# Kernel tuning notes

Measured on AMD Instinct MI355X. Metric: run time of the kernel, lower is better.

The kernel has to match this reference:

```python
import jax, jax.numpy as jnp
import numpy as np

B, S, DIN, E, M, L = 16, 4096, 64, 512, 128, 4


def _phi(u, R):
    # u: [B,S,E] (already scaled by E**-0.25), R: [E,M]
    logits = u @ R - 0.5 * jnp.sum(u * u, axis=-1, keepdims=True)
    logits = logits - jax.lax.stop_gradient(jnp.max(logits))  # constant shift cancels in num/den ratio
    return jnp.exp(logits) / np.sqrt(M).astype(np.float32)


def setup_inputs() -> dict:
    key = jax.random.key(0)
    ks = jax.random.split(key, 32)
    n = jax.random.normal
    d = {
        'x': n(ks[0], (B, S, DIN), jnp.float32),
        'Wi': n(ks[1], (DIN, E)) / np.sqrt(DIN),
        'bi': jnp.zeros((E,)),
        'pos': n(ks[2], (S, E)) * 0.02,
        'Wq': n(ks[3], (L, E, E)) / np.sqrt(E),
        'bq': jnp.zeros((L, E)),
        'Wk': n(ks[4], (L, E, E)) / np.sqrt(E),
        'bk': jnp.zeros((L, E)),
        'Wv': n(ks[5], (L, E, E)) / np.sqrt(E),
        'bv': jnp.zeros((L, E)),
        'Wo': n(ks[6], (L, E, E)) / np.sqrt(E),
        'bo': jnp.zeros((L, E)),
        'R': n(ks[7], (L, E, M)),
        'ln_g': jnp.ones((L, E)),
        'ln_b': jnp.zeros((L, E)),
        'W1': n(ks[8], (L, E, 4 * E)) / np.sqrt(E),
        'b1': jnp.zeros((L, 4 * E)),
        'W2': n(ks[9], (L, 4 * E, E)) / np.sqrt(4 * E),
        'b2': jnp.zeros((L, E)),
        'Wr1': n(ks[10], (E, E // 2)) / np.sqrt(E),
        'br1': jnp.zeros((E // 2,)),
        'Wr2': n(ks[11], (E // 2, 1)) / np.sqrt(E // 2),
        'br2': jnp.zeros((1,)),
    }
    return d


def reference(x, Wi, bi, pos, Wq, bq, Wk, bk, Wv, bv, Wo, bo, R, ln_g, ln_b, W1, b1, W2, b2, Wr1, br1, Wr2, br2):
    h = x @ Wi + bi + pos[None, :, :]  # [B,S,E]
    scale = E ** -0.25
    for i in range(L):
        residual = h
        # --- Performer linear attention (non-causal FAVOR+) ---
        q = h @ Wq[i] + bq[i]
        k = h @ Wk[i] + bk[i]
        v = h @ Wv[i] + bv[i]
        pq = _phi(q * scale, R[i])  # [B,S,M]
        pk = _phi(k * scale, R[i])  # [B,S,M]
        kv = jnp.einsum('bsm,bse->bme', pk, v)  # [B,M,E]
        z = jnp.sum(pk, axis=1)                  # [B,M]
        num = jnp.einsum('bsm,bme->bse', pq, kv)
        den = jnp.einsum('bsm,bm->bs', pq, z)[..., None]
        a = (num / (den + 1e-6)) @ Wo[i] + bo[i]
        # --- LayerNorm ---
        mu = jnp.mean(a, axis=-1, keepdims=True)
        var = jnp.var(a, axis=-1, keepdims=True)
        y = (a - mu) * jax.lax.rsqrt(var + 1e-5) * ln_g[i] + ln_b[i]
        # --- FFN (dropout is identity in eval) ---
        ff = jax.nn.gelu(y @ W1[i] + b1[i], approximate=False) @ W2[i] + b2[i]
        h = ff + residual
    pooled = h[:, 0, :]  # [B,E]
    return jax.nn.relu(pooled @ Wr1 + br1) @ Wr2 + br2  # [B,1]
```

## Files before the change

kernel.cpp:

```cpp
#include <hip/hip_runtime.h>
#include <math.h>

static constexpr int  cB   = 16;
static constexpr int  cS   = 4096;
static constexpr int  cDIN = 64;
static constexpr int  cE   = 512;
static constexpr int  cM   = 128;
static constexpr int  cL   = 4;
static constexpr int  cFF  = 2048;
static constexpr int  cHE  = 256;
static constexpr long cNBS = (long)cB * cS;
static constexpr int  cNF  = 1536;

typedef __attribute__((ext_vector_type(8))) short  bf16x8;
typedef __attribute__((ext_vector_type(4))) short  bf16x4;
typedef __attribute__((ext_vector_type(4))) float  f32x4;

typedef const __attribute__((address_space(1))) unsigned int g_u32;
typedef __attribute__((address_space(3))) unsigned int l_u32;

__device__ __forceinline__ float b2f(unsigned short u) {
  union { unsigned int i; float f; } x; x.i = ((unsigned int)u) << 16; return x.f;
}
__device__ __forceinline__ unsigned short f2b(float f) {
  union { float f; unsigned int i; } x; x.f = f;
  unsigned int r = x.i + 0x7FFFu + ((x.i >> 16) & 1u);
  return (unsigned short)(r >> 16);
}

#define PSCALE 0.21022410381342863f
#define PNRM   0.022097086912079608f
#define PINV   0.08838834764831845f

#define FLAG_BIAS    2
#define FLAG_GELU    4
#define FLAG_RES     8
#define FLAG_VT      16
#define FLAG_DEN     32
#define FLAG_RNORM   64
#define FLAG_PHIK    128
#define FLAG_F32OUT  256
#define FLAG_SPLITK8 512
#define FLAG_ATOMIC  1024
#define FLAG_FUSED   2048

#define GMT 128
#define GNT 128
#define GBK 32

__global__ __launch_bounds__(256, 2)
void gemm_kernel(const unsigned short* __restrict__ A,
                 const unsigned short* __restrict__ Bt,
                 const unsigned short* __restrict__ bias,
                 const unsigned short* __restrict__ Res,
                 const float* __restrict__ aux,
                 float* __restrict__ pmax,
                 void* __restrict__ C,
                 int K, int N, int lda, int ldb, float alpha, int flags,
                 long sA, long sB, long sC)
{
  __shared__ __align__(16) unsigned char sraw[18048];
  unsigned short (*As)[32] = (unsigned short (*)[32])sraw;
  unsigned short (*Bs)[32] = (unsigned short (*)[32])(sraw + 8192);
  unsigned short (*stage)[136] = (unsigned short (*)[136])sraw;
  float* wred  = (float*)(sraw + 17472);

  const int tid  = threadIdx.x;
  const int lane = tid & 63;
  const int wid  = tid >> 6;

  int bx = blockIdx.x, by = blockIdx.y;
  if (flags & FLAG_FUSED) { bx = blockIdx.y; by = blockIdx.x; }

  long zb = blockIdx.z;
  const long zc = blockIdx.z;
  int koff = 0;
  if (flags & FLAG_SPLITK8) { koff = (int)(zb & 7) * K; zb >>= 3; }

  const unsigned short* Ab = A + zb * sA + (long)bx * GMT * lda + koff;
  const unsigned short* Bb = Bt + zb * sB + (long)by * GNT * ldb + koff;

  const int srow = wid * 16 + (lane >> 2);
  const int scol = (lane & 3) << 3;
  const unsigned short* gA = Ab + (long)srow * lda + scol;
  const unsigned short* gB = Bb + (long)srow * ldb + scol;
  l_u32* lA0 = (l_u32*)&As[srow][scol];
  l_u32* lA1 = (l_u32*)&As[srow + 64][scol];
  l_u32* lB0 = (l_u32*)&Bs[srow][scol];
  l_u32* lB1 = (l_u32*)&Bs[srow + 64][scol];

  const f32x4 fzero = {0.f, 0.f, 0.f, 0.f};
  f32x4 acc[4][4];
#pragma unroll
  for (int i = 0; i < 4; ++i)
#pragma unroll
    for (int j = 0; j < 4; ++j) acc[i][j] = fzero;

  const int wm = (wid >> 1) << 6;
  const int wn = (wid & 1) << 6;
  const int fm = lane & 15;
  const int kq = (lane >> 4) << 3;

  const long ka64 = (long)64 * lda, kb64 = (long)64 * ldb;
  for (int k0 = 0; k0 < K; k0 += GBK) {
    __builtin_amdgcn_global_load_lds((g_u32*)(gA + k0),        lA0, 16, 0, 0);
    __builtin_amdgcn_global_load_lds((g_u32*)(gA + ka64 + k0), lA1, 16, 0, 0);
    __builtin_amdgcn_global_load_lds((g_u32*)(gB + k0),        lB0, 16, 0, 0);
    __builtin_amdgcn_global_load_lds((g_u32*)(gB + kb64 + k0), lB1, 16, 0, 0);
    __syncthreads();

    bf16x8 af[4], bfv[4];
#pragma unroll
    for (int i = 0; i < 4; ++i) {
      af[i]  = *(const bf16x8*)&As[wm + i * 16 + fm][kq];
      bfv[i] = *(const bf16x8*)&Bs[wn + i * 16 + fm][kq];
    }
#pragma unroll
    for (int i = 0; i < 4; ++i)
#pragma unroll
      for (int j = 0; j < 4; ++j)
        acc[i][j] = __builtin_amdgcn_mfma_f32_16x16x32_bf16(af[i], bfv[j], acc[i][j], 0, 0, 0);
    __syncthreads();
  }

  const int rq = (lane >> 4) << 2;
  const long crow0 = (long)bx * GMT + wm;
  const int  ccol0 = by * GNT + wn;

  long rnoff = 0;
  if (flags & FLAG_FUSED) {
    if (by < 4) flags = FLAG_BIAS | FLAG_VT;
    else { flags = FLAG_BIAS | FLAG_RNORM; if (by >= 8) rnoff = cNBS; }
  }

  if (flags & FLAG_RNORM) {
#pragma unroll
    for (int i = 0; i < 4; ++i)
#pragma unroll
      for (int r = 0; r < 4; ++r) {
        float s = 0.f;
#pragma unroll
        for (int j = 0; j < 4; ++j) {
          float v = acc[i][j][r] * alpha + b2f(bias[ccol0 + j * 16 + fm]);
          s += v * v;
        }
        s += __shfl_xor(s, 1, 64);
        s += __shfl_xor(s, 2, 64);
        s += __shfl_xor(s, 4, 64);
        s += __shfl_xor(s, 8, 64);
        if (fm == 0)
          unsafeAtomicAdd(&pmax[rnoff + crow0 + i * 16 + rq + r], s);
      }
    return;
  }

  if (flags & FLAG_PHIK) {
    const long aoff = (by == 0) ? cNBS : 0;
    float* Cf = (float*)C + (long)by * (cNBS * (long)cM);
    float mx = -3.0e38f;
#pragma unroll
    for (int i = 0; i < 4; ++i)
#pragma unroll
      for (int r = 0; r < 4; ++r) {
        const long rr = crow0 + i * 16 + rq + r;
        const float nrm = PNRM * aux[aoff + rr];
#pragma unroll
        for (int j = 0; j < 4; ++j) {
          const int cc = ccol0 + j * 16 + fm;
          const float bv = b2f(bias[cc]);
          float l = acc[i][j][r] * PSCALE + bv - nrm;
          mx = fmaxf(mx, l);
          Cf[rr * (long)cM + (cc & (cM - 1))] = l;
        }
      }
#pragma unroll
    for (int off = 32; off >= 1; off >>= 1) mx = fmaxf(mx, __shfl_down(mx, off, 64));
    if (lane == 0) wred[wid] = mx;
    __syncthreads();
    if (tid == 0)
      pmax[by * 512 + bx] = fmaxf(fmaxf(wred[0], wred[1]), fmaxf(wred[2], wred[3]));
    return;
  }

  if (flags & FLAG_ATOMIC) {
    float* Cf = (float*)C + zb * sC;
#pragma unroll
    for (int j = 0; j < 4; ++j) {
      const int cc = ccol0 + j * 16 + fm;
#pragma unroll
      for (int i = 0; i < 4; ++i)
#pragma unroll
        for (int r = 0; r < 4; ++r) {
          const long rr = crow0 + i * 16 + rq + r;
          unsafeAtomicAdd(&Cf[rr * (long)N + cc], acc[i][j][r] * alpha);
        }
    }
    return;
  }

  if (flags & FLAG_VT) {
    unsigned short* Cb = (unsigned short*)C;
    const int bb = (bx * GMT) >> 12;
    const long sbase = (long)((bx * GMT) & (cS - 1));
#pragma unroll
    for (int rnd = 0; rnd < 2; ++rnd) {
      if ((wn >> 6) == rnd) {
#pragma unroll
        for (int j = 0; j < 4; ++j) {
          const int cc = ccol0 + j * 16 + fm;
          const float bv = (flags & FLAG_BIAS) ? b2f(bias[cc]) : 0.f;
          const int cl = j * 16 + fm;
#pragma unroll
          for (int i = 0; i < 4; ++i)
#pragma unroll
            for (int r = 0; r < 4; ++r)
              stage[cl][wm + i * 16 + rq + r] = f2b(acc[i][j][r] * alpha + bv);
        }
      }
      __syncthreads();
      {
        const int cl = tid >> 2;
        const int sseg = (tid & 3) << 5;
        const int gcol = by * GNT + rnd * 64 + cl;
        unsigned short* dst = Cb + (long)bb * sC + (long)gcol * cS + sbase + sseg;
#pragma unroll
        for (int t = 0; t < 4; ++t)
          *(bf16x8*)(dst + t * 8) = *(const bf16x8*)&stage[cl][sseg + t * 8];
      }
      __syncthreads();
    }
    return;
  }

  const long rowsPerBatch = (long)gridDim.x * GMT;
#pragma unroll
  for (int j = 0; j < 4; ++j) {
    const int cc = ccol0 + j * 16 + fm;
    const float bv = (flags & FLAG_BIAS) ? b2f(bias[cc]) : 0.f;
#pragma unroll
    for (int i = 0; i < 4; ++i) {
      const long rbase = crow0 + i * 16 + rq;
#pragma unroll
      for (int r = 0; r < 4; ++r) {
        const long rr = rbase + r;
        float v = acc[i][j][r] * alpha + bv;
        if (flags & FLAG_GELU) v = 0.5f * v * (1.f + erff(v * 0.7071067811865475f));
        if (flags & FLAG_DEN)
          v *= 1.f / (fmaxf(aux[zb * rowsPerBatch + rr], 0.f) + 1e-6f);
        const long idx = zc * sC + rr * (long)N + cc;
        if (flags & FLAG_RES) v += b2f(Res[idx]);
        if (flags & FLAG_F32OUT) ((float*)C)[idx] = v;
        else                     ((unsigned short*)C)[idx] = f2b(v);
      }
    }
  }
}

__global__ void detect_kernel(const unsigned short* __restrict__ lng,
                              int* __restrict__ flag) {
  if (threadIdx.x == 0 && blockIdx.x == 0) flag[0] = (lng[0] == 0) ? 1 : 0;
}

__global__ __launch_bounds__(256) void cvt_kernel(const void* __restrict__ in,
                                                  unsigned short* __restrict__ out,
                                                  long n, const int* __restrict__ flag) {
  long i = (long)blockIdx.x * 256 + threadIdx.x;
  if (i >= n) return;
  if (flag[0]) out[i] = f2b(((const float*)in)[i]);
  else         out[i] = ((const unsigned short*)in)[i];
}

__global__ __launch_bounds__(256) void zero4_kernel(float* __restrict__ p) {
  long i = ((long)blockIdx.x * 256 + threadIdx.x) * 4;
  f32x4 z = {0.f, 0.f, 0.f, 0.f};
  *(f32x4*)&p[i] = z;
}

__global__ __launch_bounds__(256) void addpos_kernel(unsigned short* __restrict__ h,
                                                     const unsigned short* __restrict__ pos) {
  long i = ((long)blockIdx.x * 256 + threadIdx.x) * 8;
  long se = i % ((long)cS * cE);
  bf16x8 v = *(bf16x8*)&h[i];
  bf16x8 p = *(const bf16x8*)&pos[se];
#pragma unroll
  for (int r = 0; r < 8; ++r)
    v[r] = (short)f2b(b2f((unsigned short)v[r]) + b2f((unsigned short)p[r]));
  *(bf16x8*)&h[i] = v;
}

__global__ __launch_bounds__(256) void reducemax2_kernel(const float* __restrict__ partials,
                                                         float* __restrict__ gmax) {
  __shared__ float sm[8];
  const int tid = threadIdx.x;
  for (int half = 0; half < 2; ++half) {
    float mx = -3.0e38f;
    for (int i = tid; i < 512; i += 256) mx = fmaxf(mx, partials[half * 512 + i]);
#pragma unroll
    for (int off = 32; off >= 1; off >>= 1) mx = fmaxf(mx, __shfl_down(mx, off, 64));
    if ((tid & 63) == 0) sm[(half << 2) + (tid >> 6)] = mx;
  }
  __syncthreads();
  if (tid == 0) gmax[0] = fmaxf(fmaxf(sm[0], sm[1]), fmaxf(sm[2], sm[3]));
  if (tid == 1) gmax[1] = fmaxf(fmaxf(sm[4], sm[5]), fmaxf(sm[6], sm[7]));
}

__global__ __launch_bounds__(256) void expq_kernel(const float* __restrict__ lf,
                                                   const float* __restrict__ gmx,
                                                   unsigned short* __restrict__ P) {
  long i = ((long)blockIdx.x * 256 + threadIdx.x) * 4;
  const float gm = gmx[0];
  f32x4 v = *(const f32x4*)&lf[i];
  bf16x4 o;
#pragma unroll
  for (int r = 0; r < 4; ++r)
    o[r] = (short)f2b(__expf(fminf(v[r] - gm, 0.f)) * PINV);
  *(bf16x4*)&P[i] = o;
}

__global__ __launch_bounds__(256) void expT_kernel(const float* __restrict__ lf,
                                                   const float* __restrict__ gmx,
                                                   unsigned short* __restrict__ out) {
  __shared__ unsigned short t[32][33];
  const int b = blockIdx.z;
  const float gm = gmx[0];
  const int bx = blockIdx.x << 5, by = blockIdx.y << 5;
  const int tx = threadIdx.x & 31, ty = threadIdx.x >> 5;
  const float* src = lf + (long)b * cS * cM;
  unsigned short* dst = out + (long)b * cM * cS;
#pragma unroll
  for (int i = ty; i < 32; i += 8) {
    float l = src[(long)(by + i) * cM + bx + tx];
    t[i][tx] = f2b(__expf(fminf(l - gm, 0.f)) * PINV);
  }
  __syncthreads();
#pragma unroll
  for (int i = ty; i < 32; i += 8)
    dst[(long)(bx + i) * cS + by + tx] = t[tx][i];
}

__global__ __launch_bounds__(256) void kvcvt_kernel(const float* __restrict__ kvacc,
                                                    unsigned short* __restrict__ kvtb) {
  long i = ((long)blockIdx.x * 256 + threadIdx.x) * 4;
  f32x4 v = *(const f32x4*)&kvacc[i];
  bf16x4 o;
#pragma unroll
  for (int r = 0; r < 4; ++r) o[r] = (short)f2b(v[r]);
  *(bf16x4*)&kvtb[i] = o;
}

__global__ __launch_bounds__(128) void phibias_kernel(const unsigned short* __restrict__ bq,
                                                      const unsigned short* __restrict__ R,
                                                      unsigned short* __restrict__ out,
                                                      float scale, int ldo) {
  const int l = blockIdx.x, m = threadIdx.x;
  const unsigned short* b = bq + (long)l * cE;
  const unsigned short* r = R + (long)l * cE * cM;
  float a = 0.f;
  for (int e = 0; e < cE; ++e) a += b2f(b[e]) * b2f(r[(long)e * cM + m]);
  out[(long)l * ldo + m] = f2b(a * scale);
}

__global__ __launch_bounds__(256) void packb_kernel(const unsigned short* __restrict__ bv,
                                                    const unsigned short* __restrict__ bk,
                                                    const unsigned short* __restrict__ bq,
                                                    unsigned short* __restrict__ out) {
  const int l = blockIdx.x, t = threadIdx.x;
#pragma unroll
  for (int s = 0; s < 512; s += 256) {
    out[l * cNF + s + t]        = bv[l * 512 + s + t];
    out[l * cNF + 512 + s + t]  = bk[l * 512 + s + t];
    out[l * cNF + 1024 + s + t] = bq[l * 512 + s + t];
  }
}

__global__ __launch_bounds__(256) void zsumt_kernel(const unsigned short* __restrict__ qtb,
                                                    float* __restrict__ z) {
  __shared__ float sred[4];
  const int b = blockIdx.x, m = blockIdx.y, tid = threadIdx.x;
  const unsigned short* p = qtb + ((long)b * cM + m) * cS + (long)tid * 16;
  bf16x8 a = *(const bf16x8*)p;
  bf16x8 c = *(const bf16x8*)(p + 8);
  float s = 0.f;
#pragma unroll
  for (int t = 0; t < 8; ++t) s += b2f((unsigned short)a[t]) + b2f((unsigned short)c[t]);
#pragma unroll
  for (int off = 32; off >= 1; off >>= 1) s += __shfl_down(s, off, 64);
  const int w = tid >> 6, lane = tid & 63;
  if (lane == 0) sred[w] = s;
  __syncthreads();
  if (tid == 0) z[b * cM + m] = sred[0] + sred[1] + sred[2] + sred[3];
}

__global__ __launch_bounds__(256) void den_kernel(const unsigned short* __restrict__ P,
                                                  const float* __restrict__ z,
                                                  float* __restrict__ den) {
  const int w = threadIdx.x >> 6, lane = threadIdx.x & 63;
  const long row = (long)blockIdx.x * 4 + w;
  const float* zb = z + (row >> 12) * cM;
  const unsigned short* p = P + row * cM;
  float d = b2f(p[lane]) * zb[lane] + b2f(p[lane + 64]) * zb[lane + 64];
#pragma unroll
  for (int off = 32; off >= 1; off >>= 1) d += __shfl_down(d, off, 64);
  if (lane == 0) den[row] = d;
}

__global__ __launch_bounds__(256) void ln_kernel(unsigned short* __restrict__ a,
                                                 const unsigned short* __restrict__ g,
                                                 const unsigned short* __restrict__ bb) {
  __shared__ float sred[8];
  const long row = blockIdx.x;
  unsigned short* ar = a + row * cE;
  const int tid = threadIdx.x;
  float v0 = b2f(ar[tid]), v1 = b2f(ar[tid + 256]);
  float s = v0 + v1, sq = v0 * v0 + v1 * v1;
#pragma unroll
  for (int off = 32; off >= 1; off >>= 1) {
    s  += __shfl_down(s, off, 64);
    sq += __shfl_down(sq, off, 64);
  }
  const int w = tid >> 6, lane = tid & 63;
  if (lane == 0) { sred[w] = s; sred[4 + w] = sq; }
  __syncthreads();
  const float st  = sred[0] + sred[1] + sred[2] + sred[3];
  const float sqt = sred[4] + sred[5] + sred[6] + sred[7];
  const float mean = st * (1.f / 512.f);
  const float var  = fmaxf(sqt * (1.f / 512.f) - mean * mean, 0.f);
  const float rstd = rsqrtf(var + 1e-5f);
  ar[tid]       = f2b((v0 - mean) * rstd * b2f(g[tid])       + b2f(bb[tid]));
  ar[tid + 256] = f2b((v1 - mean) * rstd * b2f(g[tid + 256]) + b2f(bb[tid + 256]));
}

__global__ __launch_bounds__(256) void transpose_kernel(const unsigned short* __restrict__ in,
                                                        unsigned short* __restrict__ out,
                                                        int R, int C, long sIn, long sOut) {
  __shared__ unsigned short t[32][33];
  in  += (long)blockIdx.z * sIn;
  out += (long)blockIdx.z * sOut;
  const int bx = blockIdx.x << 5, by = blockIdx.y << 5;
  const int tx = threadIdx.x & 31, ty = threadIdx.x >> 5;
#pragma unroll
  for (int i = ty; i < 32; i += 8) t[i][tx] = in[(long)(by + i) * C + bx + tx];
  __syncthreads();
#pragma unroll
  for (int i = ty; i < 32; i += 8) out[(long)(bx + i) * R + by + tx] = t[tx][i];
}

__global__ __launch_bounds__(256) void head_kernel(const unsigned short* __restrict__ h,
                                                   const unsigned short* __restrict__ Wr1,
                                                   const unsigned short* __restrict__ br1,
                                                   const unsigned short* __restrict__ Wr2,
                                                   const unsigned short* __restrict__ br2,
                                                   void* __restrict__ out,
                                                   const int* __restrict__ flag) {
  __shared__ float pooled[cE];
  __shared__ float red[4];
  const int b = blockIdx.x, tid = threadIdx.x;
  pooled[tid]       = b2f(h[(long)b * cS * cE + tid]);
  pooled[tid + 256] = b2f(h[(long)b * cS * cE + tid + 256]);
  __syncthreads();
  float acc = b2f(br1[tid]);
  for (int e = 0; e < cE; ++e) acc += pooled[e] * b2f(Wr1[e * cHE + tid]);
  acc = fmaxf(acc, 0.f) * b2f(Wr2[tid]);
#pragma unroll
  for (int off = 32; off >= 1; off >>= 1) acc += __shfl_down(acc, off, 64);
  const int w = tid >> 6, lane = tid & 63;
  if (lane == 0) red[w] = acc;
  __syncthreads();
  if (tid == 0) {
    float r = red[0] + red[1] + red[2] + red[3] + b2f(br2[0]);
    if (flag[0]) ((float*)out)[b] = r;
    else         ((unsigned short*)out)[b] = f2b(r);
  }
}

extern "C" void kernel_launch(void* const* d_in, const int* in_sizes, int n_in,
                              void* d_out, int out_size, void* d_ws, size_t ws_size,
                              hipStream_t stream) {
  (void)in_sizes; (void)n_in; (void)out_size;

  char* ws = (char*)d_ws;
  size_t off = 0;
  auto alloc = [&](size_t bytes) -> void* {
    void* p = ws + off;
    off += (bytes + 255) & ~(size_t)255;
    return p;
  };
  unsigned short* h   = (unsigned short*)alloc(cNBS * cE * 2);
  unsigned short* X   = (unsigned short*)alloc(cNBS * cE * 2);
  unsigned short* Y   = (unsigned short*)alloc(cNBS * cE * 2);
  unsigned short* Pb  = (unsigned short*)alloc(cNBS * cM * 2);
  unsigned short* kvtb= (unsigned short*)alloc((long)cB * cE * cM * 2);
  float* kvacc        = (float*)alloc((long)cB * cE * cM * 4);
  float* vec64k       = (float*)alloc(cNBS * 4);
  float* rnorm2       = (float*)alloc(2 * cNBS * 4);
  float* z            = (float*)alloc(cB * cM * 4);
  float* partials     = (float*)alloc(1024 * 4);
  float* gmaxf        = (float*)alloc(256);
  int*   dflag        = (int*)alloc(256);
  unsigned short* WiT = (unsigned short*)alloc((long)cE * cDIN * 2);
  unsigned short* BigB= (unsigned short*)alloc((long)cL * cNF * cE * 2);
  unsigned short* BigL= (unsigned short*)alloc((long)cL * 256 * cE * 2);
  unsigned short* WoT = (unsigned short*)alloc((long)cL * cE * cE * 2);
  unsigned short* RT  = (unsigned short*)alloc((long)cL * cM * cE * 2);
  unsigned short* W1T = (unsigned short*)alloc((long)cL * cFF * cE * 2);
  unsigned short* W2T = (unsigned short*)alloc((long)cL * cE * cFF * 2);
  unsigned short* sb  = (unsigned short*)alloc(170000 * 2);

  unsigned short* WqB = X;
  unsigned short* WkB = WqB + (long)cL * cE * cE;
  unsigned short* WvB = WkB + (long)cL * cE * cE;
  unsigned short* WoB = WvB + (long)cL * cE * cE;
  unsigned short* RmB = WoB + (long)cL * cE * cE;
  unsigned short* W1B = RmB + (long)cL * cE * cM;
  unsigned short* W2B = W1B + (long)cL * cE * cFF;
  unsigned short* WiB = W2B + (long)cL * cE * cFF;
  unsigned short* xb   = Y;
  unsigned short* posb = Y + cNBS * cDIN;
  unsigned short* biC  = sb;
  unsigned short* bqC  = biC  + 512;
  unsigned short* bkC  = bqC  + 2048;
  unsigned short* bvC  = bkC  + 2048;
  unsigned short* boC  = bvC  + 2048;
  unsigned short* b1C  = boC  + 2048;
  unsigned short* b2C  = b1C  + 8192;
  unsigned short* lngC = b2C  + 2048;
  unsigned short* lnbC = lngC + 2048;
  unsigned short* Wr1C = lnbC + 2048;
  unsigned short* br1C = Wr1C + 131072;
  unsigned short* Wr2C = br1C + 256;
  unsigned short* br2C = Wr2C + 256;
  unsigned short* bqkC  = br2C + 16;
  unsigned short* b1536C = bqkC + cL * 256;

  unsigned short* qtb  = X;
  float* logfX         = (float*)X;
  unsigned short* vtb  = Y;
  unsigned short* attb = X;
  unsigned short* ab   = Y;
  unsigned short* u1b  = X;

  if (off > ws_size) return;

  detect_kernel<<<1, 64, 0, stream>>>((const unsigned short*)d_in[13], dflag);
  auto cvt = [&](const void* src, unsigned short* dst, long n) {
    cvt_kernel<<<(unsigned)((n + 255) / 256), 256, 0, stream>>>(src, dst, n, dflag);
  };
  cvt(d_in[0],  xb,   cNBS * cDIN);
  cvt(d_in[1],  WiB,  (long)cDIN * cE);
  cvt(d_in[2],  biC,  cE);
  cvt(d_in[3],  posb, (long)cS * cE);
  cvt(d_in[4],  WqB,  (long)cL * cE * cE);
  cvt(d_in[5],  bqC,  (long)cL * cE);
  cvt(d_in[6],  WkB,  (long)cL * cE * cE);
  cvt(d_in[7],  bkC,  (long)cL * cE);
  cvt(d_in[8],  WvB,  (long)cL * cE * cE);
  cvt(d_in[9],  bvC,  (long)cL * cE);
  cvt(d_in[10], WoB,  (long)cL * cE * cE);
  cvt(d_in[11], boC,  (long)cL * cE);
  cvt(d_in[12], RmB,  (long)cL * cE * cM);
  cvt(d_in[13], lngC, (long)cL * cE);
  cvt(d_in[14], lnbC, (long)cL * cE);
  cvt(d_in[15], W1B,  (long)cL * cE * cFF);
  cvt(d_in[16], b1C,  (long)cL * cFF);
  cvt(d_in[17], W2B,  (long)cL * cFF * cE);
  cvt(d_in[18], b2C,  (long)cL * cE);
  cvt(d_in[19], Wr1C, (long)cE * cHE);
  cvt(d_in[20], br1C, cHE);
  cvt(d_in[21], Wr2C, cHE);
  cvt(d_in[22], br2C, 1);

  typedef const unsigned short* cus;
  auto gemm = [&](const void* A, const void* Bt, const void* bias_,
                  const float* aux_, float* pmax_, void* C,
                  long rows, int K, int N, int lda, int ldb, float alpha, int flags,
                  long sA, long sB, long sC, int batches, const void* Res_ = nullptr) {
    dim3 g((unsigned)(rows / 128), (unsigned)(N / 128), (unsigned)batches);
    gemm_kernel<<<g, dim3(256), 0, stream>>>(
        (const unsigned short*)A, (const unsigned short*)Bt,
        (const unsigned short*)bias_, (const unsigned short*)Res_,
        aux_, pmax_, C, K, N, lda, ldb, alpha, flags, sA, sB, sC);
  };

  transpose_kernel<<<dim3(16, 2, 1), 256, 0, stream>>>(WiB, WiT, cDIN, cE, 0, 0);
  transpose_kernel<<<dim3(16, 16, cL), 256, 0, stream>>>(WvB, BigB, cE, cE, (long)cE * cE, (long)cNF * cE);
  transpose_kernel<<<dim3(16, 16, cL), 256, 0, stream>>>(WkB, BigB + (long)512 * cE, cE, cE, (long)cE * cE, (long)cNF * cE);
  transpose_kernel<<<dim3(16, 16, cL), 256, 0, stream>>>(WqB, BigB + (long)1024 * cE, cE, cE, (long)cE * cE, (long)cNF * cE);
  transpose_kernel<<<dim3(16, 16, cL), 256, 0, stream>>>(WoB, WoT, cE, cE, (long)cE * cE, (long)cE * cE);
  transpose_kernel<<<dim3(4, 16, cL), 256, 0, stream>>>(RmB, RT, cE, cM, (long)cE * cM, (long)cE * cM);
  transpose_kernel<<<dim3(64, 16, cL), 256, 0, stream>>>(W1B, W1T, cE, cFF, (long)cE * cFF, (long)cE * cFF);
  transpose_kernel<<<dim3(16, 64, cL), 256, 0, stream>>>(W2B, W2T, cFF, cE, (long)cFF * cE, (long)cFF * cE);

  gemm(RT, WqB, nullptr, nullptr, nullptr, BigL, cM, cE, cE, cE, cE, 1.f, 0,
       (long)cM * cE, (long)cE * cE, (long)256 * cE, cL);
  gemm(RT, WkB, nullptr, nullptr, nullptr, BigL + (long)128 * cE, cM, cE, cE, cE, cE, 1.f, 0,
       (long)cM * cE, (long)cE * cE, (long)256 * cE, cL);
  phibias_kernel<<<cL, 128, 0, stream>>>(bqC, RmB, bqkC, PSCALE, 256);
  phibias_kernel<<<cL, 128, 0, stream>>>(bkC, RmB, bqkC + 128, PSCALE, 256);
  packb_kernel<<<cL, 256, 0, stream>>>(bvC, bkC, bqC, b1536C);

  gemm(xb, WiT, biC, nullptr, nullptr, h, cNBS, cDIN, cE, cDIN, cDIN, 1.f,
       FLAG_BIAS, 0, 0, 0, 1);
  addpos_kernel<<<16384, 256, 0, stream>>>(h, posb);

  for (int i = 0; i < cL; ++i) {
    cus WoT_i = WoT + (long)i * cE * cE;  cus bo_i = boC + (long)i * cE;
    cus BigB_i = BigB + (long)i * cNF * cE;
    cus BigL_i = BigL + (long)i * 256 * cE;
    cus b1536_i = b1536C + (long)i * cNF;
    cus bqk_i = bqkC + (long)i * 256;
    cus g_i   = lngC + (long)i * cE;      cus b_i  = lnbC + (long)i * cE;
    cus W1T_i = W1T + (long)i * cFF * cE; cus b1_i = b1C + (long)i * cFF;
    cus W2T_i = W2T + (long)i * cE * cFF; cus b2_i = b2C + (long)i * cE;

    zero4_kernel<<<128, 256, 0, stream>>>(rnorm2);
    gemm_kernel<<<dim3(12, 512, 1), dim3(256), 0, stream>>>(
        h, BigB_i, b1536_i, nullptr, nullptr, rnorm2, vtb,
        cE, cNF, cE, cE, 1.f, FLAG_FUSED, 0, 0, (long)cE * cS);

    gemm_kernel<<<dim3(512, 2, 1), dim3(256), 0, stream>>>(
        h, BigL_i, bqk_i, nullptr, rnorm2, partials, logfX,
        cE, 256, cE, cE, PSCALE, FLAG_PHIK | FLAG_BIAS, 0, 0, 0);

    reducemax2_kernel<<<1, 256, 0, stream>>>(partials, gmaxf);
    expq_kernel<<<8192, 256, 0, stream>>>(logfX, gmaxf, Pb);
    expT_kernel<<<dim3(4, 128, cB), 256, 0, stream>>>(logfX + cNBS * cM, gmaxf + 1, qtb);

    zsumt_kernel<<<dim3(cB, cM), 256, 0, stream>>>(qtb, z);
    den_kernel<<<16384, 256, 0, stream>>>(Pb, z, vec64k);

    zero4_kernel<<<1024, 256, 0, stream>>>(kvacc);
    gemm(vtb, qtb, nullptr, nullptr, nullptr, kvacc, cE, cS / 8, cM, cS, cS, 1.f,
         FLAG_SPLITK8 | FLAG_ATOMIC, (long)cE * cS, (long)cM * cS, (long)cE * cM, cB * 8);
    kvcvt_kernel<<<1024, 256, 0, stream>>>(kvacc, kvtb);

    gemm(Pb, kvtb, nullptr, vec64k, nullptr, attb, cS, cM, cE, cM, cM, 1.f,
         FLAG_DEN, (long)cS * cM, (long)cE * cM, (long)cS * cE, cB);

    gemm(attb, WoT_i, bo_i, nullptr, nullptr, ab, cNBS, cE, cE, cE, cE, 1.f,
         FLAG_BIAS, 0, 0, 0, 1);
    ln_kernel<<<cNBS, 256, 0, stream>>>(ab, g_i, b_i);

    for (int c = 0; c < 4; ++c) {
      const unsigned short* yc = ab + (long)c * 16384 * cE;
      unsigned short* hc = h + (long)c * 16384 * cE;
      gemm(yc, W1T_i, b1_i, nullptr, nullptr, u1b, 16384, cE, cFF, cE, cE, 1.f,
           FLAG_BIAS | FLAG_GELU, 0, 0, 0, 1);
      gemm(u1b, W2T_i, b2_i, nullptr, nullptr, hc, 16384, cFF, cE, cFF, cFF, 1.f,
           FLAG_BIAS | FLAG_RES, 0, 0, 0, 1, hc);
    }
  }

  head_kernel<<<cB, 256, 0, stream>>>(h, Wr1C, br1C, Wr2C, br2C, d_out, dflag);
}
```

Measured before the change: 4.275 ms.

## Fold Wo into per-batch kv matrix and add XCD-aware block swizzle

Reassociates the attention output projection: instead of multiplying the full [B*S,E] attention result by Wo, it precomputes kv·Wo per batch ([M,E]) and applies it directly in the Pb GEMM with denominator scaling and bias. This removes one large B*S×E×E GEMM and its intermediate buffer, replacing it with a tiny per-batch GEMM. The epilogue order is changed so the denominator is applied before the bias. It also adds a block-index swizzle that groups tiles by XCD to improve L2 reuse on the big GEMMs, which risks wrong tile mapping if the grid dimensions are not divisible by 8.

Result: faster. 4.033 ms (-5.7%).

```diff
diff --git a/kernel.cpp b/kernel.cpp
--- a/kernel.cpp
+++ b/kernel.cpp
@@ -43,6 +43,7 @@
 #define FLAG_SPLITK8 512
 #define FLAG_ATOMIC  1024
 #define FLAG_FUSED   2048
+#define FLAG_SWZ     4096
 
 #define GMT 128
 #define GNT 128
@@ -70,7 +71,13 @@
   const int wid  = tid >> 6;
 
   int bx = blockIdx.x, by = blockIdx.y;
-  if (flags & FLAG_FUSED) { bx = blockIdx.y; by = blockIdx.x; }
+  if (flags & FLAG_SWZ) {
+    const unsigned lid  = blockIdx.x + gridDim.x * blockIdx.y;
+    const unsigned xcd  = lid & 7u;
+    const unsigned slot = lid >> 3;
+    bx = (int)(xcd * (gridDim.y >> 3) + slot / gridDim.x);
+    by = (int)(slot % gridDim.x);
+  }
 
   long zb = blockIdx.z;
   const long zc = blockIdx.z;
@@ -243,10 +250,11 @@
 #pragma unroll
       for (int r = 0; r < 4; ++r) {
         const long rr = rbase + r;
-        float v = acc[i][j][r] * alpha + bv;
-        if (flags & FLAG_GELU) v = 0.5f * v * (1.f + erff(v * 0.7071067811865475f));
+        float v = acc[i][j][r] * alpha;
         if (flags & FLAG_DEN)
           v *= 1.f / (fmaxf(aux[zb * rowsPerBatch + rr], 0.f) + 1e-6f);
+        v += bv;
+        if (flags & FLAG_GELU) v = 0.5f * v * (1.f + erff(v * 0.7071067811865475f));
         const long idx = zc * sC + rr * (long)N + cc;
         if (flags & FLAG_RES) v += b2f(Res[idx]);
         if (flags & FLAG_F32OUT) ((float*)C)[idx] = v;
@@ -489,8 +497,9 @@
   unsigned short* X   = (unsigned short*)alloc(cNBS * cE * 2);
   unsigned short* Y   = (unsigned short*)alloc(cNBS * cE * 2);
   unsigned short* Pb  = (unsigned short*)alloc(cNBS * cM * 2);
-  unsigned short* kvtb= (unsigned short*)alloc((long)cB * cE * cM * 2);
-  float* kvacc        = (float*)alloc((long)cB * cE * cM * 4);
+  unsigned short* kvtb= (unsigned short*)alloc((long)cB * cM * cE * 2);
+  unsigned short* kvotb=(unsigned short*)alloc((long)cB * cE * cM * 2);
+  float* kvacc        = (float*)alloc((long)cB * cM * cE * 4);
   float* vec64k       = (float*)alloc(cNBS * 4);
   float* rnorm2       = (float*)alloc(2 * cNBS * 4);
   float* z            = (float*)alloc(cB * cM * 4);
@@ -535,7 +544,6 @@
   unsigned short* qtb  = X;
   float* logfX         = (float*)X;
   unsigned short* vtb  = Y;
-  unsigned short* attb = X;
   unsigned short* ab   = Y;
   unsigned short* u1b  = X;
 
@@ -615,11 +623,11 @@
     zero4_kernel<<<128, 256, 0, stream>>>(rnorm2);
     gemm_kernel<<<dim3(12, 512, 1), dim3(256), 0, stream>>>(
         h, BigB_i, b1536_i, nullptr, nullptr, rnorm2, vtb,
-        cE, cNF, cE, cE, 1.f, FLAG_FUSED, 0, 0, (long)cE * cS);
-
-    gemm_kernel<<<dim3(512, 2, 1), dim3(256), 0, stream>>>(
+        cE, cNF, cE, cE, 1.f, FLAG_FUSED | FLAG_SWZ, 0, 0, (long)cE * cS);
+
+    gemm_kernel<<<dim3(2, 512, 1), dim3(256), 0, stream>>>(
         h, BigL_i, bqk_i, nullptr, rnorm2, partials, logfX,
-        cE, 256, cE, cE, PSCALE, FLAG_PHIK | FLAG_BIAS, 0, 0, 0);
+        cE, 256, cE, cE, PSCALE, FLAG_PHIK | FLAG_BIAS | FLAG_SWZ, 0, 0, 0);
 
     reducemax2_kernel<<<1, 256, 0, stream>>>(partials, gmaxf);
     expq_kernel<<<8192, 256, 0, stream>>>(logfX, gmaxf, Pb);
@@ -629,24 +637,26 @@
     den_kernel<<<16384, 256, 0, stream>>>(Pb, z, vec64k);
 
     zero4_kernel<<<1024, 256, 0, stream>>>(kvacc);
-    gemm(vtb, qtb, nullptr, nullptr, nullptr, kvacc, cE, cS / 8, cM, cS, cS, 1.f,
-         FLAG_SPLITK8 | FLAG_ATOMIC, (long)cE * cS, (long)cM * cS, (long)cE * cM, cB * 8);
+    gemm(qtb, vtb, nullptr, nullptr, nullptr, kvacc, cM, cS / 8, cE, cS, cS, 1.f,
+         FLAG_SPLITK8 | FLAG_ATOMIC, (long)cM * cS, (long)cE * cS, (long)cM * cE, cB * 8);
     kvcvt_kernel<<<1024, 256, 0, stream>>>(kvacc, kvtb);
 
-    gemm(Pb, kvtb, nullptr, vec64k, nullptr, attb, cS, cM, cE, cM, cM, 1.f,
-         FLAG_DEN, (long)cS * cM, (long)cE * cM, (long)cS * cE, cB);
-
-    gemm(attb, WoT_i, bo_i, nullptr, nullptr, ab, cNBS, cE, cE, cE, cE, 1.f,
-         FLAG_BIAS, 0, 0, 0, 1);
+    gemm(WoT_i, kvtb, nullptr, nullptr, nullptr, kvotb, cE, cE, cM, cE, cE, 1.f,
+         0, 0, (long)cM * cE, (long)cE * cM, cB);
+
+    gemm(Pb, kvotb, bo_i, vec64k, nullptr, ab, cS, cM, cE, cM, cM, 1.f,
+         FLAG_DEN | FLAG_BIAS, (long)cS * cM, (long)cE * cM, (long)cS * cE, cB);
     ln_kernel<<<cNBS, 256, 0, stream>>>(ab, g_i, b_i);
 
     for (int c = 0; c < 4; ++c) {
       const unsigned short* yc = ab + (long)c * 16384 * cE;
       unsigned short* hc = h + (long)c * 16384 * cE;
-      gemm(yc, W1T_i, b1_i, nullptr, nullptr, u1b, 16384, cE, cFF, cE, cE, 1.f,
-           FLAG_BIAS | FLAG_GELU, 0, 0, 0, 1);
-      gemm(u1b, W2T_i, b2_i, nullptr, nullptr, hc, 16384, cFF, cE, cFF, cFF, 1.f,
-           FLAG_BIAS | FLAG_RES, 0, 0, 0, 1, hc);
+      gemm_kernel<<<dim3(16, 128, 1), dim3(256), 0, stream>>>(
+          yc, W1T_i, b1_i, nullptr, nullptr, nullptr, u1b,
+          cE, cFF, cE, cE, 1.f, FLAG_BIAS | FLAG_GELU | FLAG_SWZ, 0, 0, 0);
+      gemm_kernel<<<dim3(4, 128, 1), dim3(256), 0, stream>>>(
+          u1b, W2T_i, b2_i, hc, nullptr, nullptr, hc,
+          cFF, cE, cFF, cFF, 1.f, FLAG_BIAS | FLAG_RES | FLAG_SWZ, 0, 0, 0);
     }
   }
 
```
